# Kernel optimization log

Measured on AMD Instinct MI355X. Metric: run time of the kernel, lower is better.

Reference implementation:

```python
import jax, jax.numpy as jnp
import numpy as np


def setup_inputs() -> dict:
    key = jax.random.key(0)
    x = jax.random.normal(key, (4, 5, 256, 32, 32), dtype=jnp.float32)
    return {"x": x, "beta": 1}


def reference(x, beta):
    # x: [B, L, D, H, W] -> [B, L, H, W, D] -> [B, L, N, D], N = H*W
    B, L, D, H, W = x.shape
    xf = jnp.transpose(x, (0, 1, 3, 4, 2)).reshape(B, L, H * W, D)
    # scores: [B, L, N, N]
    scores = jnp.einsum('blnd,blmd->blnm', xf, xf)
    # exp(beta*s)/sum == softmax(beta*s) along last axis (numerically stable form)
    attention = jax.nn.softmax(beta * scores, axis=-1)
    # (x.unsqueeze(2) * attn.unsqueeze(4)).sum(3) == attn @ x
    return jnp.einsum('blnm,blmd->blnd', attention, xf)
```

## Files before the change

kernel.cpp:

```cpp
#include <hip/hip_runtime.h>


typedef __attribute__((ext_vector_type(8))) short bf16x8;
typedef __attribute__((ext_vector_type(4))) float f32x4;
typedef __attribute__((ext_vector_type(16))) float f32x16;

#define GLD16(gp, lp) __builtin_amdgcn_global_load_lds( \
    (const __attribute__((address_space(1))) unsigned int*)(const void*)(gp), \
    (__attribute__((address_space(3))) unsigned int*)(void*)(lp), 16, 0, 0)

#define LDS_BARRIER() __asm__ volatile("s_waitcnt lgkmcnt(0)\ns_barrier" ::: "memory")
#define MEMFENCE()    __asm__ volatile("" ::: "memory")
#define WAIT_KDMA()   do { __asm__ volatile("s_waitcnt vmcnt(8)" ::: "memory"); \
                           __builtin_amdgcn_sched_barrier(0); } while (0)

__device__ __forceinline__ unsigned int pack_bf16_rne(float a, float b) {
    unsigned int ua = __float_as_uint(a); ua += 0x7FFFu + ((ua >> 16) & 1u);
    unsigned int ub = __float_as_uint(b); ub += 0x7FFFu + ((ub >> 16) & 1u);
    return (ua >> 16) | (ub & 0xFFFF0000u);
}
__device__ __forceinline__ unsigned int pack2_trunc(float lo, float hi) {
    return __builtin_amdgcn_perm(__float_as_uint(hi), __float_as_uint(lo), 0x07060302u);
}

__global__ __launch_bounds__(256) void prep_kernel(const float* __restrict__ x,
                                                   unsigned short* __restrict__ XT,
                                                   unsigned short* __restrict__ XV) {
    __shared__ __align__(16) unsigned char smem[16384];
    int bid = blockIdx.x;
    int t = threadIdx.x;
    if (bid < 640) {
        uint4* T = (uint4*)smem;
        int slice = bid >> 5, w = bid & 31;
        int cc0 = (w & 3) * 32, d0 = (w >> 2) * 32;
        const float* xs = x + slice * 262144;
        int ccl = t & 31, dr = t >> 5;
        #pragma unroll
        for (int p = 0; p < 4; ++p) {
            int dl = p * 8 + dr;
            const float* src = xs + (d0 + dl) * 1024 + (cc0 + ccl) * 8;
            float4 a = *(const float4*)(src);
            float4 b = *(const float4*)(src + 4);
            uint4 o;
            o.x = pack_bf16_rne(a.x, a.y); o.y = pack_bf16_rne(a.z, a.w);
            o.z = pack_bf16_rne(b.x, b.y); o.w = pack_bf16_rne(b.z, b.w);
            T[ccl * 32 + (dl ^ ccl)] = o;
        }
        __syncthreads();
        unsigned short* xv = XV + slice * 262144;
        int dl2 = t & 31, cr = t >> 5;
        #pragma unroll
        for (int p = 0; p < 4; ++p) {
            int ccl2 = p * 8 + cr;
            uint4 o = T[ccl2 * 32 + (dl2 ^ ccl2)];
            *(uint4*)(xv + ((cc0 + ccl2) * 256 + d0 + dl2) * 8) = o;
        }
    } else {
        unsigned long long* TX = (unsigned long long*)smem;
        int b = bid - 640;
        int slice = b >> 5, w = b & 31;
        int d0 = (w & 1) * 128, n0 = (w >> 1) * 64;
        const float* xs = x + slice * 262144;
        int nq = t & 15, dqh = t >> 4;
        #pragma unroll
        for (int p = 0; p < 2; ++p) {
            int dq = p * 16 + dqh;
            const float* src = xs + (d0 + dq * 4) * 1024 + n0 + nq * 4;
            float4 r0 = *(const float4*)(src);
            float4 r1 = *(const float4*)(src + 1024);
            float4 r2 = *(const float4*)(src + 2048);
            float4 r3 = *(const float4*)(src + 3072);
            const float* f0 = (const float*)&r0; const float* f1 = (const float*)&r1;
            const float* f2 = (const float*)&r2; const float* f3 = (const float*)&r3;
            #pragma unroll
            for (int j = 0; j < 4; ++j) {
                int nl2 = nq * 4 + j;
                unsigned long long q = (unsigned long long)pack_bf16_rne(f0[j], f1[j])
                    | ((unsigned long long)pack_bf16_rne(f2[j], f3[j]) << 32);
                TX[nl2 * 32 + (dq ^ (nl2 & 31))] = q;
            }
        }
        __syncthreads();
        unsigned short* xt = XT + slice * 262144;
        int ch = t & 15, nr = t >> 4;
        #pragma unroll
        for (int p = 0; p < 4; ++p) {
            int nl2 = p * 16 + nr;
            unsigned long long qlo = TX[nl2 * 32 + ((ch * 2) ^ (nl2 & 31))];
            unsigned long long qhi = TX[nl2 * 32 + ((ch * 2 + 1) ^ (nl2 & 31))];
            uint4 o = make_uint4((unsigned int)qlo, (unsigned int)(qlo >> 32),
                                 (unsigned int)qhi, (unsigned int)(qhi >> 32));
            *(uint4*)(xt + (n0 + nl2) * 256 + ((((d0 >> 3) + ch) ^ (nl2 & 7)) * 8)) = o;
        }
    }
}

__global__ __launch_bounds__(256, 2) void attn_kernel(const unsigned short* __restrict__ XT,
                                                      const unsigned short* __restrict__ XV,
                                                      const int* __restrict__ beta,
                                                      float* __restrict__ out) {
    __shared__ __align__(16) unsigned short Kmd[64 * 256];
    __shared__ __align__(16) unsigned short Pb[2][32 * 64];
    __shared__ float Lpart[4 * 32];
    __shared__ __align__(16) float Ltot[32];

    int bid = blockIdx.x;
    int t = ((bid & 7) * 80) + (bid >> 3);
    int slice = t >> 5, qh = t & 31;

    int tid = threadIdx.x;
    int lane = tid & 63, wv = tid >> 6;
    int nl = lane & 15, g = lane >> 4;
    int lo = lane & 31, hi = lane >> 5;

    const unsigned short* xt_s = XT + slice * 262144;
    const unsigned short* xv_s = XV + slice * 262144;
    float cscale = (float)(beta[0]) * 1.44269504089f;

    #pragma unroll
    for (int i = 0; i < 8; ++i) {
        int ch = wv * 8 + i;
        GLD16(xt_s + ch * 512 + lane * 8, &Kmd[ch * 512]);
    }
    MEMFENCE();

    bf16x8 qf[2][8];
    float mcol[2];
    #pragma unroll
    for (int nq = 0; nq < 2; ++nq) {
        int n = qh * 32 + nq * 16 + nl;
        const unsigned short* qrow = xt_s + n * 256;
        float dg = 0.f;
        #pragma unroll
        for (int ks = 0; ks < 8; ++ks) {
            qf[nq][ks] = *(const bf16x8*)(qrow + (((ks * 4 + g) ^ (n & 7)) * 8));
            const unsigned int* qu = (const unsigned int*)&qf[nq][ks];
            #pragma unroll
            for (int w = 0; w < 4; ++w) {
                float flo = __uint_as_float(qu[w] << 16);
                float fhi = __uint_as_float(qu[w] & 0xFFFF0000u);
                dg = fmaf(flo, flo, dg);
                dg = fmaf(fhi, fhi, dg);
            }
        }
        dg += __shfl_xor(dg, 16);
        dg += __shfl_xor(dg, 32);
        mcol[nq] = dg * cscale;
    }

    f32x16 acc[2];
    acc[0] = (f32x16)(0.f); acc[1] = (f32x16)(0.f);
    float lac0 = 0.f, lac1 = 0.f;

    const unsigned short* vb = xv_s + (hi * 256 + wv * 64 + lo) * 8;
    bf16x8 vf[8];
    MEMFENCE();
    #pragma unroll
    for (int ks = 0; ks < 4; ++ks) {
        vf[ks * 2]     = *(const bf16x8*)(vb + ks * 4096);
        vf[ks * 2 + 1] = *(const bf16x8*)(vb + ks * 4096 + 256);
    }

    const unsigned short* kmd_row = &Kmd[(wv * 16 + nl) * 256];

    for (int kt = 0; kt < 16; ++kt) {
        WAIT_KDMA();

        f32x4 s0 = {0.f,0.f,0.f,0.f}, s1 = {0.f,0.f,0.f,0.f};
        #pragma unroll
        for (int ks = 0; ks < 8; ++ks) {
            bf16x8 af = *(const bf16x8*)(kmd_row + (((ks * 4 + g) ^ (nl & 7)) * 8));
            s0 = __builtin_amdgcn_mfma_f32_16x16x32_bf16(af, qf[0][ks], s0, 0, 0, 0);
            s1 = __builtin_amdgcn_mfma_f32_16x16x32_bf16(af, qf[1][ks], s1, 0, 0, 0);
        }

        {
            float p0 = exp2f(fmaf(s0[0], cscale, -mcol[0]));
            float p1 = exp2f(fmaf(s0[1], cscale, -mcol[0]));
            float p2 = exp2f(fmaf(s0[2], cscale, -mcol[0]));
            float p3 = exp2f(fmaf(s0[3], cscale, -mcol[0]));
            lac0 += (p0 + p1) + (p2 + p3);
            *(uint2*)(&Pb[kt & 1][nl * 64 + (((wv * 2 + (g >> 1)) ^ (nl & 7)) * 8) + (g & 1) * 4]) =
                make_uint2(pack2_trunc(p0, p1), pack2_trunc(p2, p3));
        }
        {
            float p0 = exp2f(fmaf(s1[0], cscale, -mcol[1]));
            float p1 = exp2f(fmaf(s1[1], cscale, -mcol[1]));
            float p2 = exp2f(fmaf(s1[2], cscale, -mcol[1]));
            float p3 = exp2f(fmaf(s1[3], cscale, -mcol[1]));
            lac1 += (p0 + p1) + (p2 + p3);
            *(uint2*)(&Pb[kt & 1][(16 + nl) * 64 + (((wv * 2 + (g >> 1)) ^ (nl & 7)) * 8) + (g & 1) * 4]) =
                make_uint2(pack2_trunc(p0, p1), pack2_trunc(p2, p3));
        }

        if (kt < 15) {
            const unsigned short* gk = xt_s + (kt + 1) * 16384;
            #pragma unroll
            for (int i = 0; i < 8; ++i) {
                int ch = wv * 8 + i;
                GLD16(gk + ch * 512 + lane * 8, &Kmd[ch * 512]);
            }
        }

        LDS_BARRIER();

        {
            const unsigned short* vnext = vb + (kt + 1) * 16384;
            #pragma unroll
            for (int ks = 0; ks < 4; ++ks) {
                bf16x8 pf = *(const bf16x8*)(&Pb[kt & 1][lo * 64 + (((ks * 2 + hi) ^ (lo & 7)) * 8)]);
                acc[0] = __builtin_amdgcn_mfma_f32_32x32x16_bf16(pf, vf[ks * 2],     acc[0], 0, 0, 0);
                acc[1] = __builtin_amdgcn_mfma_f32_32x32x16_bf16(pf, vf[ks * 2 + 1], acc[1], 0, 0, 0);
                if (kt < 15) {
                    vf[ks * 2]     = *(const bf16x8*)(vnext + ks * 4096);
                    vf[ks * 2 + 1] = *(const bf16x8*)(vnext + ks * 4096 + 256);
                }
            }
        }
    }

    lac0 += __shfl_xor(lac0, 16); lac0 += __shfl_xor(lac0, 32);
    lac1 += __shfl_xor(lac1, 16); lac1 += __shfl_xor(lac1, 32);
    if (lane < 16) {
        Lpart[wv * 32 + nl] = lac0;
        Lpart[wv * 32 + 16 + nl] = lac1;
    }
    LDS_BARRIER();
    if (tid < 32)
        Ltot[tid] = 1.f / (Lpart[tid] + Lpart[32 + tid] + Lpart[64 + tid] + Lpart[96 + tid]);
    LDS_BARRIER();

    float* outs = out + slice * 262144 + (qh * 32) * 256;
    #pragma unroll
    for (int rq = 0; rq < 4; ++rq) {
        f32x4 li = *(const f32x4*)(&Ltot[rq * 8 + hi * 4]);
        #pragma unroll
        for (int j = 0; j < 4; ++j) {
            int nloc = rq * 8 + hi * 4 + j;
            #pragma unroll
            for (int db = 0; db < 2; ++db)
                outs[nloc * 256 + wv * 64 + db * 32 + lo] = acc[db][rq * 4 + j] * li[j];
        }
    }
}

extern "C" void kernel_launch(void* const* d_in, const int* in_sizes, int n_in,
                              void* d_out, int out_size, void* d_ws, size_t ws_size,
                              hipStream_t stream) {
    const float* x = (const float*)d_in[0];
    const int* beta = (const int*)d_in[1];
    float* out = (float*)d_out;
    unsigned short* XT = (unsigned short*)d_ws;
    unsigned short* XV = (unsigned short*)d_ws + 5242880;
    prep_kernel<<<1280, 256, 0, stream>>>(x, XT, XV);
    attn_kernel<<<640, 256, 0, stream>>>(XT, XV, beta, out);
}
```

Baseline: 115.7 us.

## Double query tile per block to 64 rows, staging extra queries in LDS

Each block now handles 64 query rows instead of 32, which halves the grid to 320 blocks. Each K/V tile streamed from global memory is therefore reused across twice as many queries. Three of the four 16-row query subtiles are loaded into a new LDS buffer via async global-to-LDS copies and read from LDS inside the score MFMA loop. The P buffer doubles and the row-sum scratch now aliases it. The trade-off is fewer blocks than the 256 CUs can fully occupy at two blocks per CU, plus higher LDS use and register pressure from four 32x32 accumulators.

New measurement: 118.2 us. +2.2%, slower.

```diff
diff --git a/kernel.cpp b/kernel.cpp
--- a/kernel.cpp
+++ b/kernel.cpp
@@ -100,13 +100,14 @@
                                                       const int* __restrict__ beta,
                                                       float* __restrict__ out) {
     __shared__ __align__(16) unsigned short Kmd[64 * 256];
-    __shared__ __align__(16) unsigned short Pb[2][32 * 64];
-    __shared__ float Lpart[4 * 32];
-    __shared__ __align__(16) float Ltot[32];
+    __shared__ __align__(16) unsigned short Qlds[48 * 256];
+    __shared__ __align__(16) unsigned short Pb[2][64 * 64];
+    float* Lpart = (float*)&Pb[0][0];
+    float* Ltot  = (float*)&Pb[0][2048];
 
     int bid = blockIdx.x;
-    int t = ((bid & 7) * 80) + (bid >> 3);
-    int slice = t >> 5, qh = t & 31;
+    int t = ((bid & 7) * 40) + (bid >> 3);
+    int slice = t >> 4, qh = t & 15;
 
     int tid = threadIdx.x;
     int lane = tid & 63, wv = tid >> 6;
@@ -117,24 +118,36 @@
     const unsigned short* xv_s = XV + slice * 262144;
     float cscale = (float)(beta[0]) * 1.44269504089f;
 
-    #pragma unroll
-    for (int i = 0; i < 8; ++i) {
-        int ch = wv * 8 + i;
-        GLD16(xt_s + ch * 512 + lane * 8, &Kmd[ch * 512]);
+    auto kdma = [&](int kt) {
+        const unsigned short* gk = xt_s + kt * 16384;
+        #pragma unroll
+        for (int i = 0; i < 8; ++i) {
+            int ch = wv * 8 + i;
+            GLD16(gk + ch * 512 + lane * 8, &Kmd[ch * 512]);
+        }
+    };
+
+    kdma(0);
+    {
+        const unsigned short* gq = xt_s + (qh * 64 + 16) * 256;
+        #pragma unroll
+        for (int i = 0; i < 6; ++i) {
+            int ch = wv * 6 + i;
+            GLD16(gq + ch * 512 + lane * 8, &Qlds[ch * 512]);
+        }
     }
     MEMFENCE();
 
-    bf16x8 qf[2][8];
-    float mcol[2];
-    #pragma unroll
-    for (int nq = 0; nq < 2; ++nq) {
-        int n = qh * 32 + nq * 16 + nl;
+    bf16x8 qf[8];
+    float mcol[4];
+    {
+        int n = qh * 64 + nl;
         const unsigned short* qrow = xt_s + n * 256;
         float dg = 0.f;
         #pragma unroll
         for (int ks = 0; ks < 8; ++ks) {
-            qf[nq][ks] = *(const bf16x8*)(qrow + (((ks * 4 + g) ^ (n & 7)) * 8));
-            const unsigned int* qu = (const unsigned int*)&qf[nq][ks];
+            qf[ks] = *(const bf16x8*)(qrow + (((ks * 4 + g) ^ (n & 7)) * 8));
+            const unsigned int* qu = (const unsigned int*)&qf[ks];
             #pragma unroll
             for (int w = 0; w < 4; ++w) {
                 float flo = __uint_as_float(qu[w] << 16);
@@ -145,12 +158,8 @@
         }
         dg += __shfl_xor(dg, 16);
         dg += __shfl_xor(dg, 32);
-        mcol[nq] = dg * cscale;
-    }
-
-    f32x16 acc[2];
-    acc[0] = (f32x16)(0.f); acc[1] = (f32x16)(0.f);
-    float lac0 = 0.f, lac1 = 0.f;
+        mcol[0] = dg * cscale;
+    }
 
     const unsigned short* vb = xv_s + (hi * 256 + wv * 64 + lo) * 8;
     bf16x8 vf[8];
@@ -160,47 +169,73 @@
         vf[ks * 2]     = *(const bf16x8*)(vb + ks * 4096);
         vf[ks * 2 + 1] = *(const bf16x8*)(vb + ks * 4096 + 256);
     }
+    __asm__ volatile("s_waitcnt vmcnt(8)" ::: "memory");
+    __builtin_amdgcn_sched_barrier(0);
+    LDS_BARRIER();
+
+    #pragma unroll
+    for (int st = 1; st < 4; ++st) {
+        const unsigned short* qrow = &Qlds[((st - 1) * 16 + nl) * 256];
+        float dg = 0.f;
+        #pragma unroll
+        for (int ks = 0; ks < 8; ++ks) {
+            bf16x8 qv = *(const bf16x8*)(qrow + (((ks * 4 + g) ^ (nl & 7)) * 8));
+            const unsigned int* qu = (const unsigned int*)&qv;
+            #pragma unroll
+            for (int w = 0; w < 4; ++w) {
+                float flo = __uint_as_float(qu[w] << 16);
+                float fhi = __uint_as_float(qu[w] & 0xFFFF0000u);
+                dg = fmaf(flo, flo, dg);
+                dg = fmaf(fhi, fhi, dg);
+            }
+        }
+        dg += __shfl_xor(dg, 16);
+        dg += __shfl_xor(dg, 32);
+        mcol[st] = dg * cscale;
+    }
+
+    f32x16 acc[2][2];
+    acc[0][0] = (f32x16)(0.f); acc[0][1] = (f32x16)(0.f);
+    acc[1][0] = (f32x16)(0.f); acc[1][1] = (f32x16)(0.f);
+    float lac[4] = {0.f, 0.f, 0.f, 0.f};
 
     const unsigned short* kmd_row = &Kmd[(wv * 16 + nl) * 256];
+    const unsigned short* q1 = &Qlds[nl * 256];
+    const unsigned short* q2 = &Qlds[(16 + nl) * 256];
+    const unsigned short* q3 = &Qlds[(32 + nl) * 256];
 
     for (int kt = 0; kt < 16; ++kt) {
         WAIT_KDMA();
 
         f32x4 s0 = {0.f,0.f,0.f,0.f}, s1 = {0.f,0.f,0.f,0.f};
+        f32x4 s2 = {0.f,0.f,0.f,0.f}, s3 = {0.f,0.f,0.f,0.f};
         #pragma unroll
         for (int ks = 0; ks < 8; ++ks) {
-            bf16x8 af = *(const bf16x8*)(kmd_row + (((ks * 4 + g) ^ (nl & 7)) * 8));
-            s0 = __builtin_amdgcn_mfma_f32_16x16x32_bf16(af, qf[0][ks], s0, 0, 0, 0);
-            s1 = __builtin_amdgcn_mfma_f32_16x16x32_bf16(af, qf[1][ks], s1, 0, 0, 0);
+            int ch = ((ks * 4 + g) ^ (nl & 7)) * 8;
+            bf16x8 af = *(const bf16x8*)(kmd_row + ch);
+            s0 = __builtin_amdgcn_mfma_f32_16x16x32_bf16(af, qf[ks], s0, 0, 0, 0);
+            s1 = __builtin_amdgcn_mfma_f32_16x16x32_bf16(af, *(const bf16x8*)(q1 + ch), s1, 0, 0, 0);
+            s2 = __builtin_amdgcn_mfma_f32_16x16x32_bf16(af, *(const bf16x8*)(q2 + ch), s2, 0, 0, 0);
+            s3 = __builtin_amdgcn_mfma_f32_16x16x32_bf16(af, *(const bf16x8*)(q3 + ch), s3, 0, 0, 0);
         }
 
         {
-            float p0 = exp2f(fmaf(s0[0], cscale, -mcol[0]));
-            float p1 = exp2f(fmaf(s0[1], cscale, -mcol[0]));
-            float p2 = exp2f(fmaf(s0[2], cscale, -mcol[0]));
-            float p3 = exp2f(fmaf(s0[3], cscale, -mcol[0]));
-            lac0 += (p0 + p1) + (p2 + p3);
-            *(uint2*)(&Pb[kt & 1][nl * 64 + (((wv * 2 + (g >> 1)) ^ (nl & 7)) * 8) + (g & 1) * 4]) =
-                make_uint2(pack2_trunc(p0, p1), pack2_trunc(p2, p3));
-        }
-        {
-            float p0 = exp2f(fmaf(s1[0], cscale, -mcol[1]));
-            float p1 = exp2f(fmaf(s1[1], cscale, -mcol[1]));
-            float p2 = exp2f(fmaf(s1[2], cscale, -mcol[1]));
-            float p3 = exp2f(fmaf(s1[3], cscale, -mcol[1]));
-            lac1 += (p0 + p1) + (p2 + p3);
-            *(uint2*)(&Pb[kt & 1][(16 + nl) * 64 + (((wv * 2 + (g >> 1)) ^ (nl & 7)) * 8) + (g & 1) * 4]) =
-                make_uint2(pack2_trunc(p0, p1), pack2_trunc(p2, p3));
-        }
-
-        if (kt < 15) {
-            const unsigned short* gk = xt_s + (kt + 1) * 16384;
-            #pragma unroll
-            for (int i = 0; i < 8; ++i) {
-                int ch = wv * 8 + i;
-                GLD16(gk + ch * 512 + lane * 8, &Kmd[ch * 512]);
-            }
-        }
+            f32x4 sv[4] = {s0, s1, s2, s3};
+            #pragma unroll
+            for (int st = 0; st < 4; ++st) {
+                float p0 = exp2f(fmaf(sv[st][0], cscale, -mcol[st]));
+                float p1 = exp2f(fmaf(sv[st][1], cscale, -mcol[st]));
+                float p2 = exp2f(fmaf(sv[st][2], cscale, -mcol[st]));
+                float p3 = exp2f(fmaf(sv[st][3], cscale, -mcol[st]));
+                lac[st] += (p0 + p1) + (p2 + p3);
+                *(uint2*)(&Pb[kt & 1][(st * 16 + nl) * 64 +
+                                      (((wv * 2 + (g >> 1)) ^ (nl & 7)) * 8) + (g & 1) * 4]) =
+                    make_uint2(pack2_trunc(p0, p1), pack2_trunc(p2, p3));
+            }
+        }
+
+        if (kt < 15) kdma(kt + 1);
+        MEMFENCE();
 
         LDS_BARRIER();
 
@@ -208,9 +243,13 @@
             const unsigned short* vnext = vb + (kt + 1) * 16384;
             #pragma unroll
             for (int ks = 0; ks < 4; ++ks) {
-                bf16x8 pf = *(const bf16x8*)(&Pb[kt & 1][lo * 64 + (((ks * 2 + hi) ^ (lo & 7)) * 8)]);
-                acc[0] = __builtin_amdgcn_mfma_f32_32x32x16_bf16(pf, vf[ks * 2],     acc[0], 0, 0, 0);
-                acc[1] = __builtin_amdgcn_mfma_f32_32x32x16_bf16(pf, vf[ks * 2 + 1], acc[1], 0, 0, 0);
+                int ch = ((ks * 2 + hi) ^ (lo & 7)) * 8;
+                bf16x8 pf0 = *(const bf16x8*)(&Pb[kt & 1][lo * 64 + ch]);
+                bf16x8 pf1 = *(const bf16x8*)(&Pb[kt & 1][(32 + lo) * 64 + ch]);
+                acc[0][0] = __builtin_amdgcn_mfma_f32_32x32x16_bf16(pf0, vf[ks * 2],     acc[0][0], 0, 0, 0);
+                acc[0][1] = __builtin_amdgcn_mfma_f32_32x32x16_bf16(pf0, vf[ks * 2 + 1], acc[0][1], 0, 0, 0);
+                acc[1][0] = __builtin_amdgcn_mfma_f32_32x32x16_bf16(pf1, vf[ks * 2],     acc[1][0], 0, 0, 0);
+                acc[1][1] = __builtin_amdgcn_mfma_f32_32x32x16_bf16(pf1, vf[ks * 2 + 1], acc[1][1], 0, 0, 0);
                 if (kt < 15) {
                     vf[ks * 2]     = *(const bf16x8*)(vnext + ks * 4096);
                     vf[ks * 2 + 1] = *(const bf16x8*)(vnext + ks * 4096 + 256);
@@ -219,27 +258,33 @@
         }
     }
 
-    lac0 += __shfl_xor(lac0, 16); lac0 += __shfl_xor(lac0, 32);
-    lac1 += __shfl_xor(lac1, 16); lac1 += __shfl_xor(lac1, 32);
+    #pragma unroll
+    for (int st = 0; st < 4; ++st) {
+        lac[st] += __shfl_xor(lac[st], 16);
+        lac[st] += __shfl_xor(lac[st], 32);
+    }
     if (lane < 16) {
-        Lpart[wv * 32 + nl] = lac0;
-        Lpart[wv * 32 + 16 + nl] = lac1;
+        #pragma unroll
+        for (int st = 0; st < 4; ++st) Lpart[wv * 64 + st * 16 + nl] = lac[st];
     }
     LDS_BARRIER();
-    if (tid < 32)
-        Ltot[tid] = 1.f / (Lpart[tid] + Lpart[32 + tid] + Lpart[64 + tid] + Lpart[96 + tid]);
+    if (tid < 64)
+        Ltot[tid] = 1.f / (Lpart[tid] + Lpart[64 + tid] + Lpart[128 + tid] + Lpart[192 + tid]);
     LDS_BARRIER();
 
-    float* outs = out + slice * 262144 + (qh * 32) * 256;
+    float* outs = out + slice * 262144 + (qh * 64) * 256;
     #pragma unroll
-    for (int rq = 0; rq < 4; ++rq) {
-        f32x4 li = *(const f32x4*)(&Ltot[rq * 8 + hi * 4]);
-        #pragma unroll
-        for (int j = 0; j < 4; ++j) {
-            int nloc = rq * 8 + hi * 4 + j;
-            #pragma unroll
-            for (int db = 0; db < 2; ++db)
-                outs[nloc * 256 + wv * 64 + db * 32 + lo] = acc[db][rq * 4 + j] * li[j];
+    for (int nb = 0; nb < 2; ++nb) {
+        #pragma unroll
+        for (int rq = 0; rq < 4; ++rq) {
+            f32x4 li = *(const f32x4*)(&Ltot[nb * 32 + rq * 8 + hi * 4]);
+            #pragma unroll
+            for (int j = 0; j < 4; ++j) {
+                int row = nb * 32 + rq * 8 + hi * 4 + j;
+                #pragma unroll
+                for (int dt = 0; dt < 2; ++dt)
+                    outs[row * 256 + wv * 64 + dt * 32 + lo] = acc[nb][dt][rq * 4 + j] * li[j];
+            }
         }
     }
 }
@@ -253,5 +298,5 @@
     unsigned short* XT = (unsigned short*)d_ws;
     unsigned short* XV = (unsigned short*)d_ws + 5242880;
     prep_kernel<<<1280, 256, 0, stream>>>(x, XT, XV);
-    attn_kernel<<<640, 256, 0, stream>>>(XT, XV, beta, out);
-}
+    attn_kernel<<<320, 256, 0, stream>>>(XT, XV, beta, out);
+}
```
